# Kernel optimization log

Hardware: AMD Instinct MI355X
Metric: run time of the kernel (lower is better)

Reference implementation:

```python
import jax, jax.numpy as jnp
import numpy as np

NUM_ITERATIONS = 3  # matches init kwarg num_iterations
B, R, CIN, COUT, K = 32, 2048, 64, 64, 16


def squash(s):
    # squash along the last (capsule-vector) axis, as in the torch module
    sq = jnp.sum(s * s, axis=-1, keepdims=True)
    return (sq / (1.0 + sq)) * s / jnp.sqrt(sq)


def setup_inputs() -> dict:
    key = jax.random.key(0)
    k1, k2 = jax.random.split(key)
    x = jax.random.normal(k1, (B, R, CIN), dtype=jnp.float32)
    route_weights = jax.random.normal(k2, (K, R, CIN, COUT), dtype=jnp.float32) * 0.05
    return {"x": x, "route_weights": route_weights}


def reference(x, route_weights):
    # priors[k,b,r,o] = sum_c x[b,r,c] * W[k,r,c,o]   -> [K, B, R, COUT]
    priors = jnp.einsum('brc,krco->kbro', x, route_weights)
    logits = jnp.zeros(priors.shape[:3] + (1,), dtype=priors.dtype)  # [K,B,R,1]
    outputs = None
    for i in range(NUM_ITERATIONS):
        probs = jax.nn.softmax(logits, axis=2)  # softmax over route nodes (torch dim=2)
        outputs = squash(jnp.sum(probs * priors, axis=2, keepdims=True))  # [K,B,1,COUT]
        if i != NUM_ITERATIONS - 1:
            logits = logits + jnp.sum(priors * outputs, axis=-1, keepdims=True)
    return outputs[:, :, 0, :]  # [K, B, COUT]
```

## Files before the change

kernel.cpp:

```cpp
#include <hip/hip_runtime.h>
#include <hip/hip_bf16.h>
#include <stdint.h>

#define NB 32
#define NR 2048
#define NC 64
#define NO 64
#define NK 16
#define CHC 8
#define NCHUNK (NC / CHC)

__device__ __forceinline__ uint32_t f2bf(float f) {
  uint32_t u = __builtin_bit_cast(uint32_t, f);
  return (u + 0x7fffu + ((u >> 16) & 1u)) >> 16;
}
__device__ __forceinline__ uint32_t packbf2(float lo, float hi) {
  return f2bf(lo) | (f2bf(hi) << 16);
}

__device__ __forceinline__ void gload_lds16(const float* g, float* l) {
  __builtin_amdgcn_global_load_lds(
      (const __attribute__((address_space(1))) void*)g,
      (__attribute__((address_space(3))) void*)l, 16, 0, 0);
}

__global__ __launch_bounds__(256) void transpose_x(const float* __restrict__ x,
                                                   float* __restrict__ xT) {
  __shared__ float tile[32][65];
  const int r = blockIdx.x, t = threadIdx.x;
  {
    const int b = t >> 3, c0 = (t & 7) << 3;
    const float* xp = x + ((size_t)b * NR + r) * NC + c0;
    float4 v0 = *(const float4*)xp;
    float4 v1 = *(const float4*)(xp + 4);
    tile[b][c0 + 0] = v0.x; tile[b][c0 + 1] = v0.y; tile[b][c0 + 2] = v0.z; tile[b][c0 + 3] = v0.w;
    tile[b][c0 + 4] = v1.x; tile[b][c0 + 5] = v1.y; tile[b][c0 + 6] = v1.z; tile[b][c0 + 7] = v1.w;
  }
  __syncthreads();
  {
    const int c = t >> 2, q0 = (t & 3) << 3;
    float v[8];
#pragma unroll
    for (int i = 0; i < 8; ++i) {
      const int q = q0 + i;
      v[i] = tile[(q & 3) * 8 + (q >> 2)][c];
    }
    float* op = xT + ((size_t)r * NC + c) * NB + q0;
    *(float4*)op = make_float4(v[0], v[1], v[2], v[3]);
    *(float4*)(op + 4) = make_float4(v[4], v[5], v[6], v[7]);
  }
}

__global__ __launch_bounds__(256, 3) void priors_gemm(const float* __restrict__ xT,
                                                      const float* __restrict__ W,
                                                      __hip_bfloat16* __restrict__ priors) {
  __shared__ float ldsW[2][4][CHC][64];
  __shared__ float ldsX[2][4][CHC][32];
  const int w = threadIdx.x >> 6, lane = threadIdx.x & 63;
  const int bg = lane >> 3, og = lane & 7;
  const int k = blockIdx.x & 15;
  const int rbase = (blockIdx.x >> 4) * 4;
  const int r = rbase + w;

  const float* wsrc = W + ((size_t)(k * NR + rbase + (w >> 1))) * (NC * NO)
                        + (w & 1) * 256 + lane * 4;
  const float* xsrc = xT + ((size_t)r * NC) * NB + lane * 4;

  float acc[4][8] = {};

  auto stage = [&](int t, int buf) {
    const int c0 = t * CHC;
    float* dw = &ldsW[buf][0][0][0] + w * 256;
    gload_lds16(wsrc + c0 * 64, dw);
    gload_lds16(wsrc + (size_t)2 * (NC * NO) + c0 * 64, dw + 1024);
    gload_lds16(xsrc + c0 * 32, &ldsX[buf][0][0][0] + w * 256);
  };

  auto compute = [&](int buf) {
#pragma unroll
    for (int c = 0; c < CHC; ++c) {
      float4 xv = *(const float4*)&ldsX[buf][w][c][bg * 4];
      float4 wa = *(const float4*)&ldsW[buf][w][c][og * 8];
      float4 wb = *(const float4*)&ldsW[buf][w][c][og * 8 + 4];
      float xr[4] = {xv.x, xv.y, xv.z, xv.w};
      float wr[8] = {wa.x, wa.y, wa.z, wa.w, wb.x, wb.y, wb.z, wb.w};
#pragma unroll
      for (int a = 0; a < 4; ++a)
#pragma unroll
        for (int b = 0; b < 8; ++b) acc[a][b] = fmaf(xr[a], wr[b], acc[a][b]);
    }
  };

  stage(0, 0);
  __syncthreads();
#pragma unroll
  for (int t = 0; t < NCHUNK; ++t) {
    if (t + 1 < NCHUNK) stage(t + 1, (t + 1) & 1);
    compute(t & 1);
    __syncthreads();
  }

#pragma unroll
  for (int a = 0; a < 4; ++a) {
    uint4 uv;
    uv.x = packbf2(acc[a][0], acc[a][1]);
    uv.y = packbf2(acc[a][2], acc[a][3]);
    uv.z = packbf2(acc[a][4], acc[a][5]);
    uv.w = packbf2(acc[a][6], acc[a][7]);
    __hip_bfloat16* pp = priors + ((size_t)(k * NR + r) * NB + a * 8 + bg) * NO + og * 8;
    *(uint4*)pp = uv;
  }
}

template <int PASS>
__global__ __launch_bounds__(256) void routing(const __hip_bfloat16* __restrict__ priors,
                                               float* __restrict__ Abuf,
                                               const float* __restrict__ o_prev,
                                               float* __restrict__ o_out) {
  __shared__ float o_lds[64];
  __shared__ float red_num[4][8][8];
  __shared__ float red_den[4];
  const int kb = blockIdx.x;
  const int k = kb >> 5, b = kb & 31;
  const int tid = threadIdx.x, w = tid >> 6, lane = tid & 63;
  const int g = lane >> 3, sl = lane & 7;
  const int rsub = w * 8 + g;
  const __hip_bfloat16* pbase = priors + (size_t)k * NR * NB * NO + (size_t)b * NO;
  float* ab = Abuf + (size_t)kb * NR;

  if (PASS == 1) {
    float sum[8];
#pragma unroll
    for (int j = 0; j < 8; ++j) sum[j] = 0.f;
    for (int it = 0; it < NR / 32; ++it) {
      const int r = it * 32 + rsub;
      uint4 pv = *(const uint4*)(pbase + (size_t)r * (NB * NO) + sl * 8);
      sum[0] += __builtin_bit_cast(float, pv.x << 16);
      sum[1] += __builtin_bit_cast(float, pv.x & 0xffff0000u);
      sum[2] += __builtin_bit_cast(float, pv.y << 16);
      sum[3] += __builtin_bit_cast(float, pv.y & 0xffff0000u);
      sum[4] += __builtin_bit_cast(float, pv.z << 16);
      sum[5] += __builtin_bit_cast(float, pv.z & 0xffff0000u);
      sum[6] += __builtin_bit_cast(float, pv.w << 16);
      sum[7] += __builtin_bit_cast(float, pv.w & 0xffff0000u);
    }
#pragma unroll
    for (int m = 8; m < 64; m <<= 1)
#pragma unroll
      for (int j = 0; j < 8; ++j) sum[j] += __shfl_xor(sum[j], m, 64);
    if (lane < 8) {
#pragma unroll
      for (int j = 0; j < 8; ++j) red_num[w][lane][j] = sum[j];
    }
    __syncthreads();
    if (tid < 64) {
      const int s_ = tid >> 3, j_ = tid & 7;
      float sv = (red_num[0][s_][j_] + red_num[1][s_][j_] +
                  red_num[2][s_][j_] + red_num[3][s_][j_]) * (1.f / (float)NR);
      float sq = sv * sv;
#pragma unroll
      for (int m = 1; m < 64; m <<= 1) sq += __shfl_xor(sq, m, 64);
      o_lds[tid] = (sq / (1.f + sq)) * rsqrtf(sq) * sv;
    }
    __syncthreads();
  } else {
    if (tid < 64) o_lds[tid] = o_prev[kb * 64 + tid];
    __syncthreads();
  }

  float os[8];
#pragma unroll
  for (int j = 0; j < 8; ++j) os[j] = o_lds[sl * 8 + j];

  float num[8];
#pragma unroll
  for (int j = 0; j < 8; ++j) num[j] = 0.f;
  float den = 0.f;

  for (int it = 0; it < NR / 32; ++it) {
    const int r = it * 32 + rsub;
    uint4 pv = *(const uint4*)(pbase + (size_t)r * (NB * NO) + sl * 8);
    float f[8];
    f[0] = __builtin_bit_cast(float, pv.x << 16);
    f[1] = __builtin_bit_cast(float, pv.x & 0xffff0000u);
    f[2] = __builtin_bit_cast(float, pv.y << 16);
    f[3] = __builtin_bit_cast(float, pv.y & 0xffff0000u);
    f[4] = __builtin_bit_cast(float, pv.z << 16);
    f[5] = __builtin_bit_cast(float, pv.z & 0xffff0000u);
    f[6] = __builtin_bit_cast(float, pv.w << 16);
    f[7] = __builtin_bit_cast(float, pv.w & 0xffff0000u);

    float d = 0.f;
#pragma unroll
    for (int j = 0; j < 8; ++j) d = fmaf(f[j], os[j], d);
#pragma unroll
    for (int m = 1; m < 8; m <<= 1) d += __shfl_xor(d, m, 64);

    float lg;
    if (PASS == 1) {
      lg = d;
      if (sl == 0) ab[r] = d;
    } else {
      lg = d + ab[r];
    }
    float e = __expf(lg);
    den += e;
#pragma unroll
    for (int j = 0; j < 8; ++j) num[j] = fmaf(e, f[j], num[j]);
  }

#pragma unroll
  for (int m = 8; m < 64; m <<= 1) {
    den += __shfl_xor(den, m, 64);
#pragma unroll
    for (int j = 0; j < 8; ++j) num[j] += __shfl_xor(num[j], m, 64);
  }
  if (lane < 8) {
#pragma unroll
    for (int j = 0; j < 8; ++j) red_num[w][lane][j] = num[j];
    if (lane == 0) red_den[w] = den;
  }
  __syncthreads();

  if (tid < 64) {
    const int s_ = tid >> 3, j_ = tid & 7;
    float nm = red_num[0][s_][j_] + red_num[1][s_][j_] + red_num[2][s_][j_] + red_num[3][s_][j_];
    float dn = red_den[0] + red_den[1] + red_den[2] + red_den[3];
    float sv = nm / dn;
    float sq = sv * sv;
#pragma unroll
    for (int m = 1; m < 64; m <<= 1) sq += __shfl_xor(sq, m, 64);
    float ov = (sq / (1.f + sq)) * rsqrtf(sq) * sv;
    o_out[kb * 64 + tid] = ov;
  }
}

extern "C" void kernel_launch(void* const* d_in, const int* in_sizes, int n_in,
                              void* d_out, int out_size, void* d_ws, size_t ws_size,
                              hipStream_t stream) {
  const float* x = (const float*)d_in[0];
  const float* W = (const float*)d_in[1];
  float* out = (float*)d_out;
  char* ws = (char*)d_ws;

  size_t off = 0;
  float* xT = (float*)(ws + off);                  off += (size_t)NR * NC * NB * 4;
  __hip_bfloat16* priors = (__hip_bfloat16*)(ws + off); off += (size_t)NK * NB * NR * NO * 2;
  float* o1 = (float*)(ws + off);                  off += (size_t)NK * NB * NO * 4;
  float* Abuf = (float*)(ws + off);                off += (size_t)NK * NB * NR * 4;

  transpose_x<<<NR, 256, 0, stream>>>(x, xT);
  priors_gemm<<<(NR / 4) * NK, 256, 0, stream>>>(xT, W, priors);
  routing<1><<<NK * NB, 256, 0, stream>>>(priors, Abuf, nullptr, o1);
  routing<2><<<NK * NB, 256, 0, stream>>>(priors, Abuf, o1, out);
}
```

Before: 255.1 us.

## Replace LDS-staged priors GEMM with direct global loads and register triple-buffering

```diff
diff --git a/kernel.cpp b/kernel.cpp
--- a/kernel.cpp
+++ b/kernel.cpp
@@ -7,8 +7,6 @@
 #define NC 64
 #define NO 64
 #define NK 16
-#define CHC 8
-#define NCHUNK (NC / CHC)
 
 __device__ __forceinline__ uint32_t f2bf(float f) {
   uint32_t u = __builtin_bit_cast(uint32_t, f);
@@ -16,12 +14,6 @@
 }
 __device__ __forceinline__ uint32_t packbf2(float lo, float hi) {
   return f2bf(lo) | (f2bf(hi) << 16);
-}
-
-__device__ __forceinline__ void gload_lds16(const float* g, float* l) {
-  __builtin_amdgcn_global_load_lds(
-      (const __attribute__((address_space(1))) void*)g,
-      (__attribute__((address_space(3))) void*)l, 16, 0, 0);
 }
 
 __global__ __launch_bounds__(256) void transpose_x(const float* __restrict__ x,
@@ -51,53 +43,60 @@
   }
 }
 
+#define LOADS(S, t)                                                  \
+  do {                                                               \
+    const int c0_ = (t) * 2;                                         \
+    _Pragma("unroll") for (int i = 0; i < 2; ++i) {                  \
+      wa##S[i] = *(const float4*)(wp + (c0_ + i) * NO);              \
+      wb##S[i] = *(const float4*)(wp + (c0_ + i) * NO + 4);          \
+      x##S[i]  = *(const float4*)(xp + (c0_ + i) * NB);              \
+    }                                                                \
+  } while (0)
+
+#define COMPS(S)                                                     \
+  do {                                                               \
+    _Pragma("unroll") for (int i = 0; i < 2; ++i) {                  \
+      float xr[4] = {x##S[i].x, x##S[i].y, x##S[i].z, x##S[i].w};    \
+      float wr[8] = {wa##S[i].x, wa##S[i].y, wa##S[i].z, wa##S[i].w, \
+                     wb##S[i].x, wb##S[i].y, wb##S[i].z, wb##S[i].w};\
+      _Pragma("unroll") for (int a = 0; a < 4; ++a)                  \
+        _Pragma("unroll") for (int b = 0; b < 8; ++b)                \
+          acc[a][b] = fmaf(xr[a], wr[b], acc[a][b]);                 \
+    }                                                                \
+  } while (0)
+
 __global__ __launch_bounds__(256, 3) void priors_gemm(const float* __restrict__ xT,
                                                       const float* __restrict__ W,
                                                       __hip_bfloat16* __restrict__ priors) {
-  __shared__ float ldsW[2][4][CHC][64];
-  __shared__ float ldsX[2][4][CHC][32];
   const int w = threadIdx.x >> 6, lane = threadIdx.x & 63;
   const int bg = lane >> 3, og = lane & 7;
-  const int k = blockIdx.x & 15;
-  const int rbase = (blockIdx.x >> 4) * 4;
-  const int r = rbase + w;
-
-  const float* wsrc = W + ((size_t)(k * NR + rbase + (w >> 1))) * (NC * NO)
-                        + (w & 1) * 256 + lane * 4;
-  const float* xsrc = xT + ((size_t)r * NC) * NB + lane * 4;
+  const int task = blockIdx.x * 4 + w;
+  const int k = task & 15;
+  const int r = task >> 4;
+
+  const float* wp = W + ((size_t)k * NR + r) * (NC * NO) + og * 8;
+  const float* xp = xT + (size_t)r * (NC * NB) + bg * 4;
 
   float acc[4][8] = {};
-
-  auto stage = [&](int t, int buf) {
-    const int c0 = t * CHC;
-    float* dw = &ldsW[buf][0][0][0] + w * 256;
-    gload_lds16(wsrc + c0 * 64, dw);
-    gload_lds16(wsrc + (size_t)2 * (NC * NO) + c0 * 64, dw + 1024);
-    gload_lds16(xsrc + c0 * 32, &ldsX[buf][0][0][0] + w * 256);
-  };
-
-  auto compute = [&](int buf) {
-#pragma unroll
-    for (int c = 0; c < CHC; ++c) {
-      float4 xv = *(const float4*)&ldsX[buf][w][c][bg * 4];
-      float4 wa = *(const float4*)&ldsW[buf][w][c][og * 8];
-      float4 wb = *(const float4*)&ldsW[buf][w][c][og * 8 + 4];
-      float xr[4] = {xv.x, xv.y, xv.z, xv.w};
-      float wr[8] = {wa.x, wa.y, wa.z, wa.w, wb.x, wb.y, wb.z, wb.w};
-#pragma unroll
-      for (int a = 0; a < 4; ++a)
-#pragma unroll
-        for (int b = 0; b < 8; ++b) acc[a][b] = fmaf(xr[a], wr[b], acc[a][b]);
-    }
-  };
-
-  stage(0, 0);
-  __syncthreads();
-#pragma unroll
-  for (int t = 0; t < NCHUNK; ++t) {
-    if (t + 1 < NCHUNK) stage(t + 1, (t + 1) & 1);
-    compute(t & 1);
-    __syncthreads();
+  float4 xA[2], waA[2], wbA[2];
+  float4 xB[2], waB[2], wbB[2];
+  float4 xC[2], waC[2], wbC[2];
+
+  LOADS(A, 0);
+  LOADS(B, 1);
+  LOADS(C, 2);
+#pragma unroll
+  for (int t = 0; t < 32; t += 3) {
+    COMPS(A);
+    if (t + 3 < 32) LOADS(A, t + 3);
+    if (t + 1 < 32) {
+      COMPS(B);
+      if (t + 4 < 32) LOADS(B, t + 4);
+    }
+    if (t + 2 < 32) {
+      COMPS(C);
+      if (t + 5 < 32) LOADS(C, t + 5);
+    }
   }
 
 #pragma unroll
@@ -250,7 +249,7 @@
   float* Abuf = (float*)(ws + off);                off += (size_t)NK * NB * NR * 4;
 
   transpose_x<<<NR, 256, 0, stream>>>(x, xT);
-  priors_gemm<<<(NR / 4) * NK, 256, 0, stream>>>(xT, W, priors);
+  priors_gemm<<<(NR * NK) / 4, 256, 0, stream>>>(xT, W, priors);
   routing<1><<<NK * NB, 256, 0, stream>>>(priors, Abuf, nullptr, o1);
   routing<2><<<NK * NB, 256, 0, stream>>>(priors, Abuf, o1, out);
 }
```

Measured after the change: 359.3 us. +40.8%, slower.
